# Kernel tuning notes

Hardware: AMD Instinct MI355X
Metric: run time of the kernel (lower is better)

Reference implementation:

```python
import jax, jax.numpy as jnp
import numpy as np

HEADS = 8

def setup_inputs() -> dict:
    key = jax.random.key(0)
    k1, k2, k3 = jax.random.split(key, 3)
    b, q_plus4, t, h, w, d = 4, 20, 8, 16, 16, 512
    btn_features = 512
    btn_dec = jax.random.normal(k1, (b, q_plus4, t, d), dtype=jnp.float32)
    btn_enc = jax.random.normal(k2, (b, t, h, w, d), dtype=jnp.float32)
    # nn.Linear(num_heads, btn_features): weight [out,in]; store transposed [in,out]
    W = jax.random.normal(k3, (HEADS, btn_features), dtype=jnp.float32) * (1.0 / np.sqrt(HEADS))
    bias = jnp.zeros((btn_features,), dtype=jnp.float32)
    return {"btn_dec": btn_dec, "btn_enc": btn_enc, "W": W, "bias": bias}

def reference(btn_dec, btn_enc, W, bias):
    g = HEADS
    b, t, h, w, d = btn_enc.shape
    c = d // g
    # drop last 4 queries
    dec = btn_dec[:, : btn_dec.shape[1] - 4]           # [b,q,t,d]
    q = dec.shape[1]
    dec = dec.reshape(b, q, t, g, c)                   # [b,q,t,g,c]
    enc = btn_enc.reshape(b, t, h, w, g, c)            # [b,t,h,w,g,c]
    # broadcast-multiply + channel-sum == batched contraction over c
    scores = jnp.einsum('bqtgc,bthwgc->bqthwg', dec, enc)  # [b,q,t,h,w,g]
    # MLP: Linear(g -> btn_features) + ReLU
    out = jax.nn.relu(jnp.einsum('bqthwg,gf->bqthwf', scores, W) + bias)
    return out
```

## Files before the change

### kernel.cpp

```cpp
#include <hip/hip_runtime.h>


__device__ __forceinline__ float bcast_lane(float v, int srcLane) {
    return __uint_as_float(__builtin_amdgcn_readlane(__float_as_uint(v), srcLane));
}

__global__ __launch_bounds__(256) void heatmap_kernel(
    const float* __restrict__ dec,
    const float* __restrict__ enc,
    const float* __restrict__ W,
    const float* __restrict__ bias,
    float* __restrict__ out)
{
    const int tid  = threadIdx.x;
    const int lane = tid & 63;
    const int wid  = blockIdx.x * 4 + (tid >> 6);

    const int h = wid & 15;
    const int t = (wid >> 4) & 7;
    const int q = (wid >> 7) & 15;
    const int b = wid >> 11;

    const int f0 = lane * 8;

    float4 Wr0[8], Wr1[8];
#pragma unroll
    for (int g = 0; g < 8; ++g) {
        Wr0[g] = *reinterpret_cast<const float4*>(W + g * 512 + f0);
        Wr1[g] = *reinterpret_cast<const float4*>(W + g * 512 + f0 + 4);
    }
    const float4 bi0 = *reinterpret_cast<const float4*>(bias + f0);
    const float4 bi1 = *reinterpret_cast<const float4*>(bias + f0 + 4);

    const float* decp = dec + (size_t)(((b * 20 + q) * 8 + t)) * 512 + f0;
    const float4 d0 = *reinterpret_cast<const float4*>(decp);
    const float4 d1 = *reinterpret_cast<const float4*>(decp + 4);

    const size_t ebase = (size_t)((b * 8 + t) * 256 + h * 16) * 512;
    const size_t obase = (size_t)wid * 16 * 512;

#pragma unroll 4
    for (int w = 0; w < 16; ++w) {
        const float* ep = enc + ebase + (size_t)w * 512 + f0;
        const float4 e0 = *reinterpret_cast<const float4*>(ep);
        const float4 e1 = *reinterpret_cast<const float4*>(ep + 4);

        float p = d0.x * e0.x + d0.y * e0.y + d0.z * e0.z + d0.w * e0.w
                + d1.x * e1.x + d1.y * e1.y + d1.z * e1.z + d1.w * e1.w;

        p += __shfl_xor(p, 1);
        p += __shfl_xor(p, 2);
        p += __shfl_xor(p, 4);

        float s[8];
#pragma unroll
        for (int g = 0; g < 8; ++g)
            s[g] = bcast_lane(p, g * 8);

        float4 a0 = bi0, a1 = bi1;
#pragma unroll
        for (int g = 0; g < 8; ++g) {
            a0.x += s[g] * Wr0[g].x;  a0.y += s[g] * Wr0[g].y;
            a0.z += s[g] * Wr0[g].z;  a0.w += s[g] * Wr0[g].w;
            a1.x += s[g] * Wr1[g].x;  a1.y += s[g] * Wr1[g].y;
            a1.z += s[g] * Wr1[g].z;  a1.w += s[g] * Wr1[g].w;
        }
        a0.x = fmaxf(a0.x, 0.f); a0.y = fmaxf(a0.y, 0.f);
        a0.z = fmaxf(a0.z, 0.f); a0.w = fmaxf(a0.w, 0.f);
        a1.x = fmaxf(a1.x, 0.f); a1.y = fmaxf(a1.y, 0.f);
        a1.z = fmaxf(a1.z, 0.f); a1.w = fmaxf(a1.w, 0.f);

        float* op = out + obase + (size_t)w * 512 + f0;
        *reinterpret_cast<float4*>(op)     = a0;
        *reinterpret_cast<float4*>(op + 4) = a1;
    }
}

extern "C" void kernel_launch(void* const* d_in, const int* in_sizes, int n_in,
                              void* d_out, int out_size, void* d_ws, size_t ws_size,
                              hipStream_t stream) {
    const float* dec  = (const float*)d_in[0];
    const float* enc  = (const float*)d_in[1];
    const float* W    = (const float*)d_in[2];
    const float* bias = (const float*)d_in[3];
    float* out = (float*)d_out;

    heatmap_kernel<<<2048, 256, 0, stream>>>(dec, enc, W, bias, out);
}
```

Measured before the change: 299.5 us.

## Remap waves for enc reuse, batch loads, and use nontemporal output stores

Reorders the wave index so q varies fastest, letting the 16 waves that read the same enc row run close together and hit in cache. Blocks are also swizzled across XCDs so each chiplet gets a contiguous range. Each wave now issues its enc loads and dot-reductions in two batches of eight to increase memory-level parallelism. Output is written with nontemporal stores so the write stream does not pollute cache, at the cost of more registers held live.

```diff
diff --git a/kernel.cpp b/kernel.cpp
--- a/kernel.cpp
+++ b/kernel.cpp
@@ -1,5 +1,7 @@
 #include <hip/hip_runtime.h>
 
+
+typedef float f32x4 __attribute__((ext_vector_type(4)));
 
 __device__ __forceinline__ float bcast_lane(float v, int srcLane) {
     return __uint_as_float(__builtin_amdgcn_readlane(__float_as_uint(v), srcLane));
@@ -14,65 +16,76 @@
 {
     const int tid  = threadIdx.x;
     const int lane = tid & 63;
-    const int wid  = blockIdx.x * 4 + (tid >> 6);
 
-    const int h = wid & 15;
-    const int t = (wid >> 4) & 7;
-    const int q = (wid >> 7) & 15;
+    const int bid = blockIdx.x;
+    const int sw  = (bid & 7) * 256 + (bid >> 3);
+    const int wid = sw * 4 + (tid >> 6);
+
+    const int q = wid & 15;
+    const int h = (wid >> 4) & 15;
+    const int t = (wid >> 8) & 7;
     const int b = wid >> 11;
 
     const int f0 = lane * 8;
 
-    float4 Wr0[8], Wr1[8];
+    const float* decp = dec + (size_t)((b * 20 + q) * 8 + t) * 512 + f0;
+    const f32x4 d0 = *reinterpret_cast<const f32x4*>(decp);
+    const f32x4 d1 = *reinterpret_cast<const f32x4*>(decp + 4);
+
+    f32x4 Wr0[8], Wr1[8];
 #pragma unroll
     for (int g = 0; g < 8; ++g) {
-        Wr0[g] = *reinterpret_cast<const float4*>(W + g * 512 + f0);
-        Wr1[g] = *reinterpret_cast<const float4*>(W + g * 512 + f0 + 4);
+        Wr0[g] = *reinterpret_cast<const f32x4*>(W + g * 512 + f0);
+        Wr1[g] = *reinterpret_cast<const f32x4*>(W + g * 512 + f0 + 4);
     }
-    const float4 bi0 = *reinterpret_cast<const float4*>(bias + f0);
-    const float4 bi1 = *reinterpret_cast<const float4*>(bias + f0 + 4);
+    const f32x4 bi0 = *reinterpret_cast<const f32x4*>(bias + f0);
+    const f32x4 bi1 = *reinterpret_cast<const f32x4*>(bias + f0 + 4);
 
-    const float* decp = dec + (size_t)(((b * 20 + q) * 8 + t)) * 512 + f0;
-    const float4 d0 = *reinterpret_cast<const float4*>(decp);
-    const float4 d1 = *reinterpret_cast<const float4*>(decp + 4);
+    const size_t ebase = (size_t)((b * 8 + t) * 256 + h * 16) * 512 + f0;
 
-    const size_t ebase = (size_t)((b * 8 + t) * 256 + h * 16) * 512;
-    const size_t obase = (size_t)wid * 16 * 512;
+    const int owid = ((b * 16 + q) * 8 + t) * 16 + h;
+    float* orow = out + (size_t)owid * (16 * 512) + f0;
 
-#pragma unroll 4
-    for (int w = 0; w < 16; ++w) {
-        const float* ep = enc + ebase + (size_t)w * 512 + f0;
-        const float4 e0 = *reinterpret_cast<const float4*>(ep);
-        const float4 e1 = *reinterpret_cast<const float4*>(ep + 4);
+#pragma unroll
+    for (int half = 0; half < 2; ++half) {
+        float pw[8];
+#pragma unroll
+        for (int i = 0; i < 8; ++i) {
+            const int w = half * 8 + i;
+            const float* ep = enc + ebase + (size_t)w * 512;
+            const f32x4 e0 = *reinterpret_cast<const f32x4*>(ep);
+            const f32x4 e1 = *reinterpret_cast<const f32x4*>(ep + 4);
+            float p = d0.x * e0.x + d0.y * e0.y + d0.z * e0.z + d0.w * e0.w
+                    + d1.x * e1.x + d1.y * e1.y + d1.z * e1.z + d1.w * e1.w;
+            p += __shfl_xor(p, 1);
+            p += __shfl_xor(p, 2);
+            p += __shfl_xor(p, 4);
+            pw[i] = p;
+        }
 
-        float p = d0.x * e0.x + d0.y * e0.y + d0.z * e0.z + d0.w * e0.w
-                + d1.x * e1.x + d1.y * e1.y + d1.z * e1.z + d1.w * e1.w;
+#pragma unroll
+        for (int i = 0; i < 8; ++i) {
+            const int w = half * 8 + i;
+            float sg[8];
+#pragma unroll
+            for (int g = 0; g < 8; ++g)
+                sg[g] = bcast_lane(pw[i], g * 8);
 
-        p += __shfl_xor(p, 1);
-        p += __shfl_xor(p, 2);
-        p += __shfl_xor(p, 4);
+            f32x4 a0 = bi0, a1 = bi1;
+#pragma unroll
+            for (int g = 0; g < 8; ++g) {
+                a0 += sg[g] * Wr0[g];
+                a1 += sg[g] * Wr1[g];
+            }
+            a0.x = fmaxf(a0.x, 0.f); a0.y = fmaxf(a0.y, 0.f);
+            a0.z = fmaxf(a0.z, 0.f); a0.w = fmaxf(a0.w, 0.f);
+            a1.x = fmaxf(a1.x, 0.f); a1.y = fmaxf(a1.y, 0.f);
+            a1.z = fmaxf(a1.z, 0.f); a1.w = fmaxf(a1.w, 0.f);
 
-        float s[8];
-#pragma unroll
-        for (int g = 0; g < 8; ++g)
-            s[g] = bcast_lane(p, g * 8);
-
-        float4 a0 = bi0, a1 = bi1;
-#pragma unroll
-        for (int g = 0; g < 8; ++g) {
-            a0.x += s[g] * Wr0[g].x;  a0.y += s[g] * Wr0[g].y;
-            a0.z += s[g] * Wr0[g].z;  a0.w += s[g] * Wr0[g].w;
-            a1.x += s[g] * Wr1[g].x;  a1.y += s[g] * Wr1[g].y;
-            a1.z += s[g] * Wr1[g].z;  a1.w += s[g] * Wr1[g].w;
+            float* op = orow + (size_t)w * 512;
+            __builtin_nontemporal_store(a0, reinterpret_cast<f32x4*>(op));
+            __builtin_nontemporal_store(a1, reinterpret_cast<f32x4*>(op + 4));
         }
-        a0.x = fmaxf(a0.x, 0.f); a0.y = fmaxf(a0.y, 0.f);
-        a0.z = fmaxf(a0.z, 0.f); a0.w = fmaxf(a0.w, 0.f);
-        a1.x = fmaxf(a1.x, 0.f); a1.y = fmaxf(a1.y, 0.f);
-        a1.z = fmaxf(a1.z, 0.f); a1.w = fmaxf(a1.w, 0.f);
-
-        float* op = out + obase + (size_t)w * 512 + f0;
-        *reinterpret_cast<float4*>(op)     = a0;
-        *reinterpret_cast<float4*>(op + 4) = a1;
     }
 }
 
```

After: 338.1 us. 1.13x slower.
